# Optimization experiments

Hardware: AMD Instinct MI355X
Metric: run time of the kernel (lower is better)

The kernel has to match this reference:

```python
import jax, jax.numpy as jnp
import numpy as np

N_HEAD = 8
D_HEAD = 64
D_MODEL = 512
CTX = 64
B = 2
Q_LEN = 2048
T = Q_LEN + CTX - 1


def setup_inputs() -> dict:
    key = jax.random.key(0)
    ks = jax.random.split(key, 7)
    HD = N_HEAD * D_HEAD
    return {
        "x": jax.random.normal(ks[0], (B, T, D_MODEL), jnp.float32),
        "r": jax.random.normal(ks[1], (CTX, D_MODEL), jnp.float32),
        "Wkv": jax.random.normal(ks[2], (D_MODEL, 2 * HD), jnp.float32) * 0.02,
        "Wq": jax.random.normal(ks[3], (D_MODEL, HD), jnp.float32) * 0.02,
        "bq": jax.random.normal(ks[4], (HD,), jnp.float32) * 0.02,
        "Wr": jax.random.normal(ks[5], (D_MODEL, HD), jnp.float32) * 0.02,
        "Wo": jax.random.normal(ks[6], (HD, D_MODEL), jnp.float32) * 0.02,
    }


def reference(x, r, Wkv, Wq, bq, Wr, Wo):
    Bb, Tt, _ = x.shape
    C = r.shape[0]
    H, Dh = N_HEAD, D_HEAD
    q_len = Tt - C + 1
    scale = Dh ** -0.5

    kv = x @ Wkv                                  # [B, T, 2*H*Dh]
    k_all = kv[..., : H * Dh].reshape(Bb, Tt, H, Dh)
    v_all = kv[..., H * Dh:].reshape(Bb, Tt, H, Dh)

    # sliding windows (torch unfold(1, ctx, 1) equivalent)
    idx = jnp.arange(q_len)[:, None] + jnp.arange(C)[None, :]   # [q, C]
    k_win = k_all[:, idx]                         # [B, q, C, H, Dh]
    v_win = v_all[:, idx]                         # [B, q, C, H, Dh]

    hq = (x[:, C - 1:] @ Wq + bq).reshape(Bb, q_len, H, Dh)     # [B, q, H, Dh]
    hr = (r @ Wr).reshape(C, H, Dh)                              # [C, H, Dh]

    # q . (k + r): split into content term + relative-position bias term
    scores = (jnp.einsum('bqhd,bqchd->bhqc', hq, k_win)
              + jnp.einsum('bqhd,chd->bhqc', hq, hr)) * scale    # [B, H, q, C]

    # padding mask: positions in first ctx-1 steps that are all-zero
    pad_mask = jnp.all(x[:, : C - 1] == 0, axis=-1)              # [B, C-1]
    full_mask = jnp.concatenate(
        [pad_mask, jnp.zeros((Bb, q_len), dtype=bool)], axis=1)  # [B, T]
    mask_win = full_mask[:, idx]                                 # [B, q, C]
    scores = jnp.where(mask_win[:, None], -jnp.inf, scores)

    w = jax.nn.softmax(scores, axis=-1)                          # [B, H, q, C]
    out = jnp.einsum('bhqc,bqchd->bqhd', w, v_win).reshape(Bb, q_len, H * Dh)
    return out @ Wo                                              # [B, q, d_model]
```

## Files before the change

kernel.cpp:

```cpp
#include <hip/hip_runtime.h>
#include <cstdint>
#include <cstddef>

#define NH 8
#define DH 64
#define DM 512
#define CTX 64
#define BB 2
#define QL 2048
#define TT (QL + CTX - 1)
#define HDIM 512
#define KVN 1024
#define KD 512

typedef unsigned short u16;
typedef __attribute__((ext_vector_type(8))) short bf16x8;
typedef __attribute__((ext_vector_type(4))) float f32x4;

__device__ __forceinline__ u16 f2bf(float f) {
    uint32_t u = __float_as_uint(f);
    u += 0x7FFF + ((u >> 16) & 1);
    return (u16)(u >> 16);
}
__device__ __forceinline__ float bf2f(u16 u) {
    return __uint_as_float((uint32_t)u << 16);
}

#define GLLDS(g, l) __builtin_amdgcn_global_load_lds( \
    (const __attribute__((address_space(1))) void*)(g), \
    (__attribute__((address_space(3))) void*)(l), 16, 0, 0)

__global__ __launch_bounds__(256) void prep_kernel(
    const float* __restrict__ x, const float* __restrict__ r,
    const float* __restrict__ Wkv, const float* __restrict__ Wq,
    const float* __restrict__ Wr, const float* __restrict__ Wo,
    u16* __restrict__ xb, u16* __restrict__ rb, u16* __restrict__ WkvqT,
    u16* __restrict__ WrT, u16* __restrict__ WoT, float* __restrict__ maskv)
{
    __shared__ float tile[64][65];
    __shared__ int anyflag;
    int bid = blockIdx.x;
    const int tid = threadIdx.x;

    if (bid < 2111) {
        int i = bid * 256 + tid;
        float4 v = ((const float4*)x)[i];
        ushort4 o; o.x = f2bf(v.x); o.y = f2bf(v.y); o.z = f2bf(v.z); o.w = f2bf(v.w);
        ((ushort4*)xb)[i] = o;
        return;
    }
    bid -= 2111;
    if (bid < 32) {
        int i = bid * 256 + tid;
        float4 v = ((const float4*)r)[i];
        ushort4 o; o.x = f2bf(v.x); o.y = f2bf(v.y); o.z = f2bf(v.z); o.w = f2bf(v.w);
        ((ushort4*)rb)[i] = o;
        return;
    }
    bid -= 32;
    if (bid >= 320) {
        int idx = bid - 320;
        int t = idx >> 1, b = idx & 1;
        const float* row = x + (size_t)(b * TT + t) * DM;
        bool nz = (row[tid] != 0.f) || (row[tid + 256] != 0.f);
        if (tid == 0) anyflag = 0;
        __syncthreads();
        unsigned long long bal = __ballot(nz);
        if ((tid & 63) == 0 && bal) atomicOr(&anyflag, 1);
        __syncthreads();
        if (tid == 0) maskv[b * 64 + t] = anyflag ? 0.f : -1e30f;
        return;
    }
    const float* W; u16* WT; int N; int tidx;
    if (bid < 128)      { W = Wkv; WT = WkvqT;                    N = 1024; tidx = bid; }
    else if (bid < 192) { W = Wq;  WT = WkvqT + (size_t)1024*512; N = 512;  tidx = bid - 128; }
    else if (bid < 256) { W = Wr;  WT = WrT;                      N = 512;  tidx = bid - 192; }
    else                { W = Wo;  WT = WoT;                      N = 512;  tidx = bid - 256; }
    const int tpr = N / 64;
    const int kb = (tidx / tpr) * 64, nb = (tidx % tpr) * 64;
    const int c4 = (tid & 15) * 4;
    for (int kk = tid >> 4; kk < 64; kk += 16) {
        float4 v = *(const float4*)&W[(size_t)(kb + kk) * N + nb + c4];
        tile[kk][c4 + 0] = v.x; tile[kk][c4 + 1] = v.y;
        tile[kk][c4 + 2] = v.z; tile[kk][c4 + 3] = v.w;
    }
    __syncthreads();
    for (int nn = tid >> 4; nn < 64; nn += 16) {
        ushort4 o;
        o.x = f2bf(tile[c4 + 0][nn]); o.y = f2bf(tile[c4 + 1][nn]);
        o.z = f2bf(tile[c4 + 2][nn]); o.w = f2bf(tile[c4 + 3][nn]);
        *(ushort4*)&WT[(size_t)(nb + nn) * KD + kb + c4] = o;
    }
}

__global__ __launch_bounds__(256) void gemm_mfma(
    const u16* __restrict__ A, const u16* __restrict__ BT,
    u16* __restrict__ C, u16* __restrict__ C2, const float* __restrict__ bq,
    int mode)
{
    __shared__ u16 As[128 * 32];
    __shared__ u16 Bs[128 * 32];

    const int tid  = threadIdx.x;
    const int lane = tid & 63;
    const int w    = tid >> 6;
    const int wm   = (w >> 1) * 64;
    const int wn   = (w & 1) * 64;
    const int m0   = blockIdx.y * 128;
    const int n0   = blockIdx.x * 128;

    const int am0 = tid >> 2;
    const int ak0 = (tid & 3) * 8;
    const u16* ga0 = A  + (size_t)(m0 + am0) * KD + ak0;
    const u16* ga1 = ga0 + (size_t)64 * KD;
    const u16* gb0 = BT + (size_t)(n0 + am0) * KD + ak0;
    const u16* gb1 = gb0 + (size_t)64 * KD;

    f32x4 acc[4][4];
#pragma unroll
    for (int i = 0; i < 4; i++)
#pragma unroll
        for (int j = 0; j < 4; j++)
            acc[i][j] = (f32x4){0.f, 0.f, 0.f, 0.f};

    for (int kt = 0; kt < KD; kt += 32) {
        __syncthreads();
        GLLDS(ga0 + kt, &As[(size_t)w * 512]);
        GLLDS(ga1 + kt, &As[2048 + (size_t)w * 512]);
        GLLDS(gb0 + kt, &Bs[(size_t)w * 512]);
        GLLDS(gb1 + kt, &Bs[2048 + (size_t)w * 512]);
        __syncthreads();

        const int fm = lane & 15;
        const int fk = (lane >> 4) * 8;
        bf16x8 af[4], bfr[4];
#pragma unroll
        for (int i = 0; i < 4; i++)
            af[i] = *(const bf16x8*)&As[(wm + i * 16 + fm) * 32 + fk];
#pragma unroll
        for (int j = 0; j < 4; j++)
            bfr[j] = *(const bf16x8*)&Bs[(wn + j * 16 + fm) * 32 + fk];
#pragma unroll
        for (int i = 0; i < 4; i++)
#pragma unroll
            for (int j = 0; j < 4; j++)
                acc[i][j] = __builtin_amdgcn_mfma_f32_16x16x32_bf16(af[i], bfr[j], acc[i][j], 0, 0, 0);
    }

    const int fc = lane & 15;
    const int fr = (lane >> 4) * 4;
    if (mode == 1) {
        const bool iskv = (n0 < 1024);
#pragma unroll
        for (int i = 0; i < 4; i++)
#pragma unroll
            for (int rr = 0; rr < 4; rr++) {
                int row = m0 + wm + i * 16 + fr + rr;
                if (row < BB * TT) {
                    if (iskv) {
#pragma unroll
                        for (int j = 0; j < 4; j++) {
                            int col = n0 + wn + j * 16 + fc;
                            C[(size_t)row * KVN + col] = f2bf(acc[i][j][rr]);
                        }
                    } else {
                        int bb = row / TT;
                        int t  = row - bb * TT;
                        if (t >= CTX - 1) {
                            size_t orow = (size_t)(bb * QL + t - (CTX - 1));
#pragma unroll
                            for (int j = 0; j < 4; j++) {
                                int col = n0 + wn + j * 16 + fc - 1024;
                                C2[orow * HDIM + col] = f2bf(acc[i][j][rr] + bq[col]);
                            }
                        }
                    }
                }
            }
    } else {
#pragma unroll
        for (int i = 0; i < 4; i++)
#pragma unroll
            for (int rr = 0; rr < 4; rr++) {
                int row = m0 + wm + i * 16 + fr + rr;
                if (row < CTX) {
#pragma unroll
                    for (int j = 0; j < 4; j++) {
                        int col = n0 + wn + j * 16 + fc;
                        C[(size_t)row * HDIM + col] = f2bf(acc[i][j][rr]);
                    }
                }
            }
    }
}

__global__ __launch_bounds__(256) void gemm_n64(
    const u16* __restrict__ A, const u16* __restrict__ BT,
    float* __restrict__ C, int M, int N)
{
    __shared__ u16 As[128 * 32];
    __shared__ u16 Bs[64 * 32];

    const int tid  = threadIdx.x;
    const int lane = tid & 63;
    const int w    = tid >> 6;
    const int wm   = (w >> 1) * 64;
    const int wn   = (w & 1) * 32;
    const int m0   = blockIdx.y * 128;
    const int n0   = blockIdx.x * 64;

    const int am0 = tid >> 2;
    const int ak0 = (tid & 3) * 8;
    const u16* ga0 = A  + (size_t)(m0 + am0) * KD + ak0;
    const u16* ga1 = ga0 + (size_t)64 * KD;
    const u16* gb0 = BT + (size_t)(n0 + am0) * KD + ak0;

    f32x4 acc[4][2];
#pragma unroll
    for (int i = 0; i < 4; i++)
#pragma unroll
        for (int j = 0; j < 2; j++)
            acc[i][j] = (f32x4){0.f, 0.f, 0.f, 0.f};

    for (int kt = 0; kt < KD; kt += 32) {
        __syncthreads();
        GLLDS(ga0 + kt, &As[(size_t)w * 512]);
        GLLDS(ga1 + kt, &As[2048 + (size_t)w * 512]);
        GLLDS(gb0 + kt, &Bs[(size_t)w * 512]);
        __syncthreads();

        const int fm = lane & 15;
        const int fk = (lane >> 4) * 8;
        bf16x8 af[4], bfr[2];
#pragma unroll
        for (int i = 0; i < 4; i++)
            af[i] = *(const bf16x8*)&As[(wm + i * 16 + fm) * 32 + fk];
#pragma unroll
        for (int j = 0; j < 2; j++)
            bfr[j] = *(const bf16x8*)&Bs[(wn + j * 16 + fm) * 32 + fk];
#pragma unroll
        for (int i = 0; i < 4; i++)
#pragma unroll
            for (int j = 0; j < 2; j++)
                acc[i][j] = __builtin_amdgcn_mfma_f32_16x16x32_bf16(af[i], bfr[j], acc[i][j], 0, 0, 0);
    }

    const int fc = lane & 15;
    const int fr = (lane >> 4) * 4;
#pragma unroll
    for (int i = 0; i < 4; i++)
#pragma unroll
        for (int rr = 0; rr < 4; rr++) {
            int row = m0 + wm + i * 16 + fr + rr;
            if (row < M) {
#pragma unroll
                for (int j = 0; j < 2; j++) {
                    int col = n0 + wn + j * 16 + fc;
                    C[(size_t)row * N + col] = acc[i][j][rr];
                }
            }
        }
}

__global__ __launch_bounds__(256) void attn_mfma(
    const u16* __restrict__ kvb, const u16* __restrict__ hqb,
    const u16* __restrict__ hrb, const float* __restrict__ maskv,
    u16* __restrict__ attnb)
{
    __shared__ __align__(16) char lds[55296];
    float* sprime = (float*)lds;
    u16*   vTs    = (u16*)lds;
    float* s2s    = (float*)(lds + 20480);
    u16*   wband  = (u16*)(lds + 37888);

    const int q0 = blockIdx.x * 64;
    const int h  = blockIdx.y;
    const int b  = blockIdx.z;
    const int tid  = threadIdx.x;
    const int lane = tid & 63;
    const int w    = tid >> 6;
    const int qb   = q0 + w * 16;

    {
        uint32_t* wz = (uint32_t*)wband;
#pragma unroll
        for (int i = 0; i < 17; i++) wz[tid + i * 256] = 0;
    }
    __syncthreads();

    const int fm = lane & 15;
    const int fk = (lane >> 4) * 8;

    const u16* hqrow = hqb + (size_t)(b * QL + qb + fm) * HDIM + h * DH + fk;
    bf16x8 afr0 = *(const bf16x8*)(hqrow);
    bf16x8 afr1 = *(const bf16x8*)(hqrow + 32);

    {
        const u16* kbase = kvb + (size_t)(b * TT + qb + fm) * KVN + h * DH + fk;
#pragma unroll
        for (int nt = 0; nt < 5; nt++) {
            bf16x8 b0 = *(const bf16x8*)(kbase + (size_t)nt * 16 * KVN);
            bf16x8 b1 = *(const bf16x8*)(kbase + (size_t)nt * 16 * KVN + 32);
            f32x4 acc = (f32x4){0.f, 0.f, 0.f, 0.f};
            acc = __builtin_amdgcn_mfma_f32_16x16x32_bf16(afr0, b0, acc, 0, 0, 0);
            acc = __builtin_amdgcn_mfma_f32_16x16x32_bf16(afr1, b1, acc, 0, 0, 0);
            const int row = (lane >> 4) * 4;
#pragma unroll
            for (int r = 0; r < 4; r++)
                sprime[w * 1280 + (row + r) * 80 + nt * 16 + fm] = acc[r];
        }
    }
    {
        const u16* hrbase = hrb + (size_t)fm * HDIM + h * DH + fk;
#pragma unroll
        for (int nc = 0; nc < 4; nc++) {
            bf16x8 b0 = *(const bf16x8*)(hrbase + (size_t)nc * 16 * HDIM);
            bf16x8 b1 = *(const bf16x8*)(hrbase + (size_t)nc * 16 * HDIM + 32);
            f32x4 acc = (f32x4){0.f, 0.f, 0.f, 0.f};
            acc = __builtin_amdgcn_mfma_f32_16x16x32_bf16(afr0, b0, acc, 0, 0, 0);
            acc = __builtin_amdgcn_mfma_f32_16x16x32_bf16(afr1, b1, acc, 0, 0, 0);
            const int row = (lane >> 4) * 4;
#pragma unroll
            for (int r = 0; r < 4; r++)
                s2s[w * 1088 + (row + r) * 68 + nc * 16 + fm] = acc[r];
        }
    }

#pragma unroll 1
    for (int i = 0; i < 16; i++) {
        const int qloc = w * 16 + i;
        float s = (sprime[w * 1280 + i * 80 + i + lane] +
                   s2s[w * 1088 + i * 68 + lane]) * 0.125f;
        if (q0 == 0) {
            int t = qloc + lane;
            if (t < 63) s += maskv[b * 64 + t];
        }
        float mx = s;
#pragma unroll
        for (int off = 32; off; off >>= 1) mx = fmaxf(mx, __shfl_xor(mx, off, 64));
        float e = __expf(s - mx);
        float sum = e;
#pragma unroll
        for (int off = 32; off; off >>= 1) sum += __shfl_xor(sum, off, 64);
        wband[qloc * 136 + qloc + lane] = f2bf(e / sum);
    }
    __syncthreads();

    {
        const int r0 = tid >> 4;
        const int c4 = (tid & 15) * 4;
        for (int rr = r0; rr < 127; rr += 16) {
            ushort4 vv = *(const ushort4*)&kvb[(size_t)(b * TT + q0 + rr) * KVN + HDIM + h * DH + c4];
            vTs[(c4 + 0) * 136 + rr] = vv.x;
            vTs[(c4 + 1) * 136 + rr] = vv.y;
            vTs[(c4 + 2) * 136 + rr] = vv.z;
            vTs[(c4 + 3) * 136 + rr] = vv.w;
        }
        if (tid < 64) vTs[tid * 136 + 127] = 0;
    }
    __syncthreads();

    f32x4 oacc[4];
#pragma unroll
    for (int j = 0; j < 4; j++) oacc[j] = (f32x4){0.f, 0.f, 0.f, 0.f};
#pragma unroll
    for (int ks = 0; ks < 4; ks++) {
        bf16x8 wa = *(const bf16x8*)&wband[(w * 16 + fm) * 136 + ks * 32 + fk];
#pragma unroll
        for (int j = 0; j < 4; j++) {
            bf16x8 vb = *(const bf16x8*)&vTs[(j * 16 + fm) * 136 + ks * 32 + fk];
            oacc[j] = __builtin_amdgcn_mfma_f32_16x16x32_bf16(wa, vb, oacc[j], 0, 0, 0);
        }
    }
    {
        const int row = (lane >> 4) * 4;
#pragma unroll
        for (int j = 0; j < 4; j++)
#pragma unroll
            for (int r = 0; r < 4; r++)
                attnb[(size_t)(b * QL + qb + row + r) * HDIM + h * DH + j * 16 + fm] =
                    f2bf(oacc[j][r]);
    }
}

extern "C" void kernel_launch(void* const* d_in, const int* in_sizes, int n_in,
                              void* d_out, int out_size, void* d_ws, size_t ws_size,
                              hipStream_t stream)
{
    const float* x   = (const float*)d_in[0];
    const float* r   = (const float*)d_in[1];
    const float* Wkv = (const float*)d_in[2];
    const float* Wq  = (const float*)d_in[3];
    const float* bq  = (const float*)d_in[4];
    const float* Wr  = (const float*)d_in[5];
    const float* Wo  = (const float*)d_in[6];
    float* out = (float*)d_out;

    char* p = (char*)d_ws;
    u16* xb     = (u16*)p;  p += (size_t)4224 * 512 * 2;
    u16* rb     = (u16*)p;  p += (size_t)128 * 512 * 2;
    u16* WkvqT  = (u16*)p;  p += (size_t)1536 * 512 * 2;
    u16* WrT    = (u16*)p;  p += (size_t)512 * 512 * 2;
    u16* WoT    = (u16*)p;  p += (size_t)512 * 512 * 2;
    u16* kvb    = (u16*)p;  p += (size_t)4224 * 1024 * 2;
    u16* hqb    = (u16*)p;  p += (size_t)4096 * 512 * 2;
    u16* hrb    = (u16*)p;  p += (size_t)64 * 512 * 2;
    u16* attnb  = (u16*)p;  p += (size_t)4096 * 512 * 2;
    float* maskv = (float*)p;

    hipLaunchKernelGGL(prep_kernel, dim3(2589), dim3(256), 0, stream,
                       x, r, Wkv, Wq, Wr, Wo, xb, rb, WkvqT, WrT, WoT, maskv);
    hipLaunchKernelGGL(gemm_mfma, dim3(1536 / 128, 33), dim3(256), 0, stream,
                       xb, WkvqT, kvb, hqb, bq, 1);
    hipLaunchKernelGGL(gemm_mfma, dim3(512 / 128, 1), dim3(256), 0, stream,
                       rb, WrT, hrb, nullptr, nullptr, 2);
    hipLaunchKernelGGL(attn_mfma, dim3(QL / 64, NH, BB), dim3(256), 0, stream,
                       kvb, hqb, hrb, maskv, attnb);
    hipLaunchKernelGGL(gemm_n64, dim3(512 / 64, 4096 / 128), dim3(256), 0, stream,
                       attnb, WoT, out, 4096, 512);
}
```

Measured before the change: 133.6 us.

## Fuse projection GEMMs, double-buffer GEMM LDS, and prefetch V in attention

```diff
diff --git a/kernel.cpp b/kernel.cpp
--- a/kernel.cpp
+++ b/kernel.cpp
@@ -21,9 +21,6 @@
     uint32_t u = __float_as_uint(f);
     u += 0x7FFF + ((u >> 16) & 1);
     return (u16)(u >> 16);
-}
-__device__ __forceinline__ float bf2f(u16 u) {
-    return __uint_as_float((uint32_t)u << 16);
 }
 
 #define GLLDS(g, l) __builtin_amdgcn_global_load_lds( \
@@ -93,21 +90,27 @@
     }
 }
 
-__global__ __launch_bounds__(256) void gemm_mfma(
-    const u16* __restrict__ A, const u16* __restrict__ BT,
-    u16* __restrict__ C, u16* __restrict__ C2, const float* __restrict__ bq,
-    int mode)
+__global__ __launch_bounds__(256) void gemm_fused(
+    const u16* __restrict__ xb, const u16* __restrict__ WkvqT,
+    u16* __restrict__ kvb, u16* __restrict__ hqb, const float* __restrict__ bq,
+    const u16* __restrict__ rb, const u16* __restrict__ WrT,
+    u16* __restrict__ hrb)
 {
-    __shared__ u16 As[128 * 32];
-    __shared__ u16 Bs[128 * 32];
+    __shared__ u16 As[2][128 * 32];
+    __shared__ u16 Bs[2][128 * 32];
 
     const int tid  = threadIdx.x;
     const int lane = tid & 63;
     const int w    = tid >> 6;
     const int wm   = (w >> 1) * 64;
     const int wn   = (w & 1) * 64;
-    const int m0   = blockIdx.y * 128;
-    const int n0   = blockIdx.x * 128;
+
+    const int bid = blockIdx.x;
+    const bool g3 = (bid >= 396);
+    const u16* A;  const u16* BT;
+    int m0, n0;
+    if (g3) { A = rb; BT = WrT;   m0 = 0;                n0 = (bid - 396) * 128; }
+    else    { A = xb; BT = WkvqT; m0 = (bid / 12) * 128; n0 = (bid % 12) * 128; }
 
     const int am0 = tid >> 2;
     const int ak0 = (tid & 3) * 8;
@@ -116,6 +119,13 @@
     const u16* gb0 = BT + (size_t)(n0 + am0) * KD + ak0;
     const u16* gb1 = gb0 + (size_t)64 * KD;
 
+#define STAGE_G1(buf, kt) do { \
+    GLLDS(ga0 + (kt), &As[buf][(size_t)w * 512]); \
+    GLLDS(ga1 + (kt), &As[buf][2048 + (size_t)w * 512]); \
+    GLLDS(gb0 + (kt), &Bs[buf][(size_t)w * 512]); \
+    GLLDS(gb1 + (kt), &Bs[buf][2048 + (size_t)w * 512]); \
+} while (0)
+
     f32x4 acc[4][4];
 #pragma unroll
     for (int i = 0; i < 4; i++)
@@ -123,33 +133,36 @@
         for (int j = 0; j < 4; j++)
             acc[i][j] = (f32x4){0.f, 0.f, 0.f, 0.f};
 
+    STAGE_G1(0, 0);
+    __syncthreads();
+
+    int cur = 0;
+    const int fm = lane & 15;
+    const int fk = (lane >> 4) * 8;
     for (int kt = 0; kt < KD; kt += 32) {
-        __syncthreads();
-        GLLDS(ga0 + kt, &As[(size_t)w * 512]);
-        GLLDS(ga1 + kt, &As[2048 + (size_t)w * 512]);
-        GLLDS(gb0 + kt, &Bs[(size_t)w * 512]);
-        GLLDS(gb1 + kt, &Bs[2048 + (size_t)w * 512]);
-        __syncthreads();
-
-        const int fm = lane & 15;
-        const int fk = (lane >> 4) * 8;
+        if (kt + 32 < KD) STAGE_G1(cur ^ 1, kt + 32);
+
         bf16x8 af[4], bfr[4];
 #pragma unroll
         for (int i = 0; i < 4; i++)
-            af[i] = *(const bf16x8*)&As[(wm + i * 16 + fm) * 32 + fk];
+            af[i] = *(const bf16x8*)&As[cur][(wm + i * 16 + fm) * 32 + fk];
 #pragma unroll
         for (int j = 0; j < 4; j++)
-            bfr[j] = *(const bf16x8*)&Bs[(wn + j * 16 + fm) * 32 + fk];
+            bfr[j] = *(const bf16x8*)&Bs[cur][(wn + j * 16 + fm) * 32 + fk];
 #pragma unroll
         for (int i = 0; i < 4; i++)
 #pragma unroll
             for (int j = 0; j < 4; j++)
                 acc[i][j] = __builtin_amdgcn_mfma_f32_16x16x32_bf16(af[i], bfr[j], acc[i][j], 0, 0, 0);
-    }
+
+        __syncthreads();
+        cur ^= 1;
+    }
+#undef STAGE_G1
 
     const int fc = lane & 15;
     const int fr = (lane >> 4) * 4;
-    if (mode == 1) {
+    if (!g3) {
         const bool iskv = (n0 < 1024);
 #pragma unroll
         for (int i = 0; i < 4; i++)
@@ -161,7 +174,7 @@
 #pragma unroll
                         for (int j = 0; j < 4; j++) {
                             int col = n0 + wn + j * 16 + fc;
-                            C[(size_t)row * KVN + col] = f2bf(acc[i][j][rr]);
+                            kvb[(size_t)row * KVN + col] = f2bf(acc[i][j][rr]);
                         }
                     } else {
                         int bb = row / TT;
@@ -171,7 +184,7 @@
 #pragma unroll
                             for (int j = 0; j < 4; j++) {
                                 int col = n0 + wn + j * 16 + fc - 1024;
-                                C2[orow * HDIM + col] = f2bf(acc[i][j][rr] + bq[col]);
+                                hqb[orow * HDIM + col] = f2bf(acc[i][j][rr] + bq[col]);
                             }
                         }
                     }
@@ -187,7 +200,7 @@
 #pragma unroll
                     for (int j = 0; j < 4; j++) {
                         int col = n0 + wn + j * 16 + fc;
-                        C[(size_t)row * HDIM + col] = f2bf(acc[i][j][rr]);
+                        hrb[(size_t)row * HDIM + col] = f2bf(acc[i][j][rr]);
                     }
                 }
             }
@@ -198,8 +211,8 @@
     const u16* __restrict__ A, const u16* __restrict__ BT,
     float* __restrict__ C, int M, int N)
 {
-    __shared__ u16 As[128 * 32];
-    __shared__ u16 Bs[64 * 32];
+    __shared__ u16 As[2][128 * 32];
+    __shared__ u16 Bs[2][64 * 32];
 
     const int tid  = threadIdx.x;
     const int lane = tid & 63;
@@ -215,6 +228,12 @@
     const u16* ga1 = ga0 + (size_t)64 * KD;
     const u16* gb0 = BT + (size_t)(n0 + am0) * KD + ak0;
 
+#define STAGE_G2(buf, kt) do { \
+    GLLDS(ga0 + (kt), &As[buf][(size_t)w * 512]); \
+    GLLDS(ga1 + (kt), &As[buf][2048 + (size_t)w * 512]); \
+    GLLDS(gb0 + (kt), &Bs[buf][(size_t)w * 512]); \
+} while (0)
+
     f32x4 acc[4][2];
 #pragma unroll
     for (int i = 0; i < 4; i++)
@@ -222,28 +241,32 @@
         for (int j = 0; j < 2; j++)
             acc[i][j] = (f32x4){0.f, 0.f, 0.f, 0.f};
 
+    STAGE_G2(0, 0);
+    __syncthreads();
+
+    int cur = 0;
+    const int fm = lane & 15;
+    const int fk = (lane >> 4) * 8;
     for (int kt = 0; kt < KD; kt += 32) {
-        __syncthreads();
-        GLLDS(ga0 + kt, &As[(size_t)w * 512]);
-        GLLDS(ga1 + kt, &As[2048 + (size_t)w * 512]);
-        GLLDS(gb0 + kt, &Bs[(size_t)w * 512]);
-        __syncthreads();
-
-        const int fm = lane & 15;
-        const int fk = (lane >> 4) * 8;
+        if (kt + 32 < KD) STAGE_G2(cur ^ 1, kt + 32);
+
         bf16x8 af[4], bfr[2];
 #pragma unroll
         for (int i = 0; i < 4; i++)
-            af[i] = *(const bf16x8*)&As[(wm + i * 16 + fm) * 32 + fk];
+            af[i] = *(const bf16x8*)&As[cur][(wm + i * 16 + fm) * 32 + fk];
 #pragma unroll
         for (int j = 0; j < 2; j++)
-            bfr[j] = *(const bf16x8*)&Bs[(wn + j * 16 + fm) * 32 + fk];
+            bfr[j] = *(const bf16x8*)&Bs[cur][(wn + j * 16 + fm) * 32 + fk];
 #pragma unroll
         for (int i = 0; i < 4; i++)
 #pragma unroll
             for (int j = 0; j < 2; j++)
                 acc[i][j] = __builtin_amdgcn_mfma_f32_16x16x32_bf16(af[i], bfr[j], acc[i][j], 0, 0, 0);
-    }
+
+        __syncthreads();
+        cur ^= 1;
+    }
+#undef STAGE_G2
 
     const int fc = lane & 15;
     const int fr = (lane >> 4) * 4;
@@ -269,8 +292,7 @@
 {
     __shared__ __align__(16) char lds[55296];
     float* sprime = (float*)lds;
-    u16*   vTs    = (u16*)lds;
-    float* s2s    = (float*)(lds + 20480);
+    u16*   vTs    = (u16*)(lds + 20480);
     u16*   wband  = (u16*)(lds + 37888);
 
     const int q0 = blockIdx.x * 64;
@@ -281,12 +303,25 @@
     const int w    = tid >> 6;
     const int qb   = q0 + w * 16;
 
+    const int vr0 = tid >> 4;
+    const int vc4 = (tid & 15) * 4;
+    ushort4 vreg[8];
+#pragma unroll
+    for (int i = 0; i < 8; i++) {
+        int rr = vr0 + i * 16;
+        if (rr < 127)
+            vreg[i] = *(const ushort4*)&kvb[(size_t)(b * TT + q0 + rr) * KVN + HDIM + h * DH + vc4];
+        else
+            vreg[i] = (ushort4){0, 0, 0, 0};
+    }
+
     {
         uint32_t* wz = (uint32_t*)wband;
 #pragma unroll
         for (int i = 0; i < 17; i++) wz[tid + i * 256] = 0;
     }
-    __syncthreads();
+    asm volatile("s_waitcnt lgkmcnt(0)" ::: "memory");
+    __builtin_amdgcn_s_barrier();
 
     const int fm = lane & 15;
     const int fk = (lane >> 4) * 8;
@@ -322,15 +357,23 @@
             const int row = (lane >> 4) * 4;
 #pragma unroll
             for (int r = 0; r < 4; r++)
-                s2s[w * 1088 + (row + r) * 68 + nc * 16 + fm] = acc[r];
+                sprime[w * 1280 + (row + r) * 81 + nc * 16 + fm] += acc[r];
         }
+    }
+
+#pragma unroll
+    for (int i = 0; i < 8; i++) {
+        int rr = vr0 + i * 16;
+        vTs[(vc4 + 0) * 136 + rr] = vreg[i].x;
+        vTs[(vc4 + 1) * 136 + rr] = vreg[i].y;
+        vTs[(vc4 + 2) * 136 + rr] = vreg[i].z;
+        vTs[(vc4 + 3) * 136 + rr] = vreg[i].w;
     }
 
 #pragma unroll 1
     for (int i = 0; i < 16; i++) {
         const int qloc = w * 16 + i;
-        float s = (sprime[w * 1280 + i * 80 + i + lane] +
-                   s2s[w * 1088 + i * 68 + lane]) * 0.125f;
+        float s = sprime[w * 1280 + i * 81 + lane] * 0.125f;
         if (q0 == 0) {
             int t = qloc + lane;
             if (t < 63) s += maskv[b * 64 + t];
@@ -343,20 +386,6 @@
 #pragma unroll
         for (int off = 32; off; off >>= 1) sum += __shfl_xor(sum, off, 64);
         wband[qloc * 136 + qloc + lane] = f2bf(e / sum);
-    }
-    __syncthreads();
-
-    {
-        const int r0 = tid >> 4;
-        const int c4 = (tid & 15) * 4;
-        for (int rr = r0; rr < 127; rr += 16) {
-            ushort4 vv = *(const ushort4*)&kvb[(size_t)(b * TT + q0 + rr) * KVN + HDIM + h * DH + c4];
-            vTs[(c4 + 0) * 136 + rr] = vv.x;
-            vTs[(c4 + 1) * 136 + rr] = vv.y;
-            vTs[(c4 + 2) * 136 + rr] = vv.z;
-            vTs[(c4 + 3) * 136 + rr] = vv.w;
-        }
-        if (tid < 64) vTs[tid * 136 + 127] = 0;
     }
     __syncthreads();
 
@@ -410,10 +439,8 @@
 
     hipLaunchKernelGGL(prep_kernel, dim3(2589), dim3(256), 0, stream,
                        x, r, Wkv, Wq, Wr, Wo, xb, rb, WkvqT, WrT, WoT, maskv);
-    hipLaunchKernelGGL(gemm_mfma, dim3(1536 / 128, 33), dim3(256), 0, stream,
-                       xb, WkvqT, kvb, hqb, bq, 1);
-    hipLaunchKernelGGL(gemm_mfma, dim3(512 / 128, 1), dim3(256), 0, stream,
-                       rb, WrT, hrb, nullptr, nullptr, 2);
+    hipLaunchKernelGGL(gemm_fused, dim3(400), dim3(256), 0, stream,
+                       xb, WkvqT, kvb, hqb, bq, rb, WrT, hrb);
     hipLaunchKernelGGL(attn_mfma, dim3(QL / 64, NH, BB), dim3(256), 0, stream,
                        kvb, hqb, hrb, maskv, attnb);
     hipLaunchKernelGGL(gemm_n64, dim3(512 / 64, 4096 / 128), dim3(256), 0, stream,
```

Result: faster. 124.8 us (-6.5%).
